# Performance work log

Hardware: AMD Instinct MI355X
Metric: run time of the kernel (lower is better)

Reference implementation:

```python
import jax, jax.numpy as jnp
import numpy as np

NUM_EMBEDDINGS = 1024
EMBEDDING_DIM = 256


def setup_inputs() -> dict:
    key = jax.random.key(0)
    k_in, k_w = jax.random.split(key)
    inputs = jax.random.normal(k_in, (32, EMBEDDING_DIM, 2048), dtype=jnp.float32)
    # nn.Embedding weight initialized uniform in [-1/K, 1/K]
    bound = 1.0 / NUM_EMBEDDINGS
    weight = jax.random.uniform(k_w, (NUM_EMBEDDINGS, EMBEDDING_DIM),
                                dtype=jnp.float32, minval=-bound, maxval=bound)
    return {"inputs": inputs, "weight": weight}


def reference(inputs, weight):
    B, D, T = inputs.shape
    # [B, D, T] -> [B*T, D]
    flat = jnp.transpose(inputs, (0, 2, 1)).reshape(-1, D)
    distances = (jnp.sum(flat * flat, axis=1, keepdims=True)
                 + jnp.sum(weight * weight, axis=1)
                 - 2.0 * flat @ weight.T)  # [N, K]
    encoding_indices = jnp.argmin(distances, axis=1)  # [N]
    # one-hot @ weight is just a gather
    quantized = weight[encoding_indices].reshape(B, T, D)  # [B, T, D]
    quantized = jnp.transpose(quantized, (0, 2, 1))  # [B, D, T]
    # straight-through estimator
    quantized = inputs + jax.lax.stop_gradient(quantized - inputs)
    return quantized, encoding_indices[:, None]
```

## Files before the change

kernel.cpp:

```cpp
#include <hip/hip_runtime.h>


#define VQ_B   32
#define VQ_D   256
#define VQ_T   2048
#define VQ_K   1024

typedef _Float16 f16x8 __attribute__((ext_vector_type(8)));
typedef float    f32x4 __attribute__((ext_vector_type(4)));

#define GLOAD_LDS16(gaddr, laddr) \
  __builtin_amdgcn_global_load_lds((const __attribute__((address_space(1))) void*)(gaddr), \
                                   (__attribute__((address_space(3))) void*)(laddr), 16, 0, 0)

__global__ void vq_wprep_kernel(const float* __restrict__ w,
                                float* __restrict__ wnorm,
                                _Float16* __restrict__ Wh,
                                _Float16* __restrict__ Wl) {
    const int k = blockIdx.x * 256 + threadIdx.x;
    const float4* wr = (const float4*)(w + (size_t)k * VQ_D);
    double s = 0.0;
    for (int i = 0; i < VQ_D / 4; ++i) {
        float4 v = wr[i];
        s += (double)v.x * v.x + (double)v.y * v.y
           + (double)v.z * v.z + (double)v.w * v.w;
        const float e4[4] = {v.x, v.y, v.z, v.w};
        #pragma unroll
        for (int j = 0; j < 4; ++j) {
            const float es = e4[j] * 1024.0f;
            const _Float16 h = (_Float16)es;
            const _Float16 l = (_Float16)((es - (float)h) * 16777216.0f);
            Wh[(size_t)k * VQ_D + i * 4 + j] = h;
            Wl[(size_t)k * VQ_D + i * 4 + j] = l;
        }
    }
    wnorm[k] = (float)s;
}

__global__ __launch_bounds__(256) void vq_xprep_kernel(
    const float* __restrict__ inp,
    _Float16* __restrict__ Xh, _Float16* __restrict__ Xl,
    float* __restrict__ xnorm)
{
    __shared__ double ps[128];
    const int tid  = threadIdx.x;
    const int t    = tid & 127;
    const int half = tid >> 7;
    const int b    = blockIdx.x >> 4;
    const int tg   = (blockIdx.x & 15) * 128 + t;
    const float* p = inp + (size_t)b * VQ_D * VQ_T + tg;

    double s = 0.0;
    for (int dc = half * 16; dc < half * 16 + 16; ++dc) {
        float x[8];
        #pragma unroll
        for (int j = 0; j < 8; ++j)
            x[j] = p[(size_t)(dc * 8 + j) * VQ_T];
        f16x8 hv, lv;
        #pragma unroll
        for (int j = 0; j < 8; ++j) {
            s += (double)x[j] * (double)x[j];
            const _Float16 h = (_Float16)x[j];
            hv[j] = h;
            lv[j] = (_Float16)((x[j] - (float)h) * 16777216.0f);
        }
        const size_t off = (((size_t)b * 32 + dc) * VQ_T + tg) * 8;
        *(f16x8*)(Xh + off) = hv;
        *(f16x8*)(Xl + off) = lv;
    }
    if (half) ps[t] = s;
    __syncthreads();
    if (!half) xnorm[(size_t)b * VQ_T + tg] = (float)(s + ps[t]);
}

__global__ __launch_bounds__(256, 2) void vq_mfma_kernel(
    const _Float16* __restrict__ Wh, const _Float16* __restrict__ Wl,
    const _Float16* __restrict__ Xh, const _Float16* __restrict__ Xl,
    const float* __restrict__ wnorm, const float* __restrict__ xnorm,
    const float* __restrict__ w,
    float* __restrict__ outq, float* __restrict__ outi)
{
    __shared__ alignas(16) char stg[2][32768];
    const int tid  = threadIdx.x;
    const int lane = tid & 63;
    const int wv   = tid >> 6;
    const int m16  = lane & 15;
    const int quad = lane >> 4;
    const int wm   = wv & 1;
    const int wn   = wv >> 1;
    const int b    = blockIdx.x >> 4;
    const int tt0  = (blockIdx.x & 15) * 128;
    const long bt  = (long)b * VQ_T + tt0;

    float xnr[4];
    #pragma unroll
    for (int fn = 0; fn < 4; ++fn)
        xnr[fn] = xnorm[bt + wn * 64 + fn * 16 + m16];

    const char* gp[8];
    #pragma unroll
    for (int i = 0; i < 8; ++i) {
        const int hf = i >> 2, f = i & 3;
        if (wv < 2) {
            const char* baseW = (const char*)((wv & 1) ? Wl : Wh);
            gp[i] = baseW + (size_t)(hf * 64 + f * 16 + m16) * 512 + quad * 16;
        } else {
            const char* baseX = (const char*)((wv & 1) ? Xl : Xh);
            gp[i] = baseX + (((size_t)b * 32 + quad) * 2048
                             + (tt0 + hf * 64 + f * 16 + m16)) * 16;
        }
    }
    auto advance = [&](int q) {
        if ((q & 7) == 7) {
            #pragma unroll
            for (int i = 0; i < 8; ++i)
                gp[i] += (wv < 2) ? (long)(65536 - 448) : (long)(-7) * 131072;
        } else {
            #pragma unroll
            for (int i = 0; i < 8; ++i)
                gp[i] += (wv < 2) ? 64L : 131072L;
        }
    };

    float bestv[4] = {3.0e38f, 3.0e38f, 3.0e38f, 3.0e38f};
    int   besti[4] = {0, 0, 0, 0};
    f32x4 acch[4][4], accl[4][4];

    #pragma unroll
    for (int i = 0; i < 8; ++i)
        GLOAD_LDS16(gp[i], &stg[0][(wv * 8 + i) * 1024]);
    advance(0);

    for (int s = 0; s < 64; ++s) {
        const int cur = s & 1;
        if ((s & 7) == 0) {
            #pragma unroll
            for (int fm = 0; fm < 4; ++fm)
                #pragma unroll
                for (int fn = 0; fn < 4; ++fn) {
                    acch[fm][fn] = (f32x4){0.f, 0.f, 0.f, 0.f};
                    accl[fm][fn] = (f32x4){0.f, 0.f, 0.f, 0.f};
                }
        }
        __syncthreads();
        if (s < 63) {
            #pragma unroll
            for (int i = 0; i < 8; ++i)
                GLOAD_LDS16(gp[i], &stg[cur ^ 1][(wv * 8 + i) * 1024]);
            advance(s + 1);
        }

        const char* base = stg[cur];
        f16x8 ah[4], al[4], bh[4], bl[4];
        #pragma unroll
        for (int f = 0; f < 4; ++f) {
            ah[f] = *(const f16x8*)(base + ((wm * 4 + f)) * 1024 + lane * 16);
            al[f] = *(const f16x8*)(base + ((8 + wm * 4 + f)) * 1024 + lane * 16);
            bh[f] = *(const f16x8*)(base + ((16 + wn * 4 + f)) * 1024 + lane * 16);
            bl[f] = *(const f16x8*)(base + ((24 + wn * 4 + f)) * 1024 + lane * 16);
        }
        #pragma unroll
        for (int fm = 0; fm < 4; ++fm)
            #pragma unroll
            for (int fn = 0; fn < 4; ++fn) {
                acch[fm][fn] = __builtin_amdgcn_mfma_f32_16x16x32_f16(
                    ah[fm], bh[fn], acch[fm][fn], 0, 0, 0);
                accl[fm][fn] = __builtin_amdgcn_mfma_f32_16x16x32_f16(
                    ah[fm], bl[fn], accl[fm][fn], 0, 0, 0);
                accl[fm][fn] = __builtin_amdgcn_mfma_f32_16x16x32_f16(
                    al[fm], bh[fn], accl[fm][fn], 0, 0, 0);
            }

        if ((s & 7) == 7) {
            const int k0 = (s >> 3) * 128;
            #pragma unroll
            for (int fm = 0; fm < 4; ++fm) {
                #pragma unroll
                for (int r = 0; r < 4; ++r) {
                    const int kg = k0 + wm * 64 + fm * 16 + quad * 4 + r;
                    const float wnk = wnorm[kg];
                    #pragma unroll
                    for (int fn = 0; fn < 4; ++fn) {
                        const float t1 = xnr[fn] + wnk;
                        const float d2 = (acch[fm][fn][r]
                                          + accl[fm][fn][r] * 5.9604644775390625e-8f)
                                         * 0.001953125f;
                        const float sc = t1 - d2;
                        if (sc < bestv[fn]) { bestv[fn] = sc; besti[fn] = kg; }
                    }
                }
            }
        }
    }

    float rv[4]; int ri[4];
    #pragma unroll
    for (int fn = 0; fn < 4; ++fn) {
        float bv = bestv[fn]; int bi = besti[fn];
        #pragma unroll
        for (int mask = 16; mask <= 32; mask <<= 1) {
            const float ov = __shfl_xor(bv, mask, 64);
            const int   oi = __shfl_xor(bi, mask, 64);
            if (ov < bv || (ov == bv && oi < bi)) { bv = ov; bi = oi; }
        }
        rv[fn] = bv; ri[fn] = bi;
    }

    __syncthreads();
    float* sv = (float*)stg[0];
    int*   si = (int*)(stg[0] + 1024);
    if (quad == 0) {
        #pragma unroll
        for (int fn = 0; fn < 4; ++fn) {
            const int tl = wn * 64 + fn * 16 + m16;
            sv[wm * 128 + tl] = rv[fn];
            si[wm * 128 + tl] = ri[fn];
        }
    }
    __syncthreads();
    if (tid < 128) {
        const float v0 = sv[tid], v1 = sv[128 + tid];
        const int   i0 = si[tid], i1 = si[128 + tid];
        const int   bi = (v1 < v0 || (v1 == v0 && i1 < i0)) ? i1 : i0;
        si[tid] = bi;
        outi[bt + tid] = (float)bi;
    }
    __syncthreads();

    {
        const int t  = tid & 127;
        const int dh = tid >> 7;
        const int bi = si[t];
        const float* wrow = w + (size_t)bi * VQ_D + dh * 128;
        float* obase = outq + ((size_t)b * VQ_D + (size_t)dh * 128) * VQ_T + tt0 + t;
        #pragma unroll 4
        for (int dd = 0; dd < 128; dd += 4) {
            float4 v = *(const float4*)(wrow + dd);
            obase[(size_t)(dd + 0) * VQ_T] = v.x;
            obase[(size_t)(dd + 1) * VQ_T] = v.y;
            obase[(size_t)(dd + 2) * VQ_T] = v.z;
            obase[(size_t)(dd + 3) * VQ_T] = v.w;
        }
    }
}

extern "C" void kernel_launch(void* const* d_in, const int* in_sizes, int n_in,
                              void* d_out, int out_size, void* d_ws, size_t ws_size,
                              hipStream_t stream) {
    const float* inp = (const float*)d_in[0];
    const float* w   = (const float*)d_in[1];
    float* outq  = (float*)d_out;
    float* outi  = outq + (size_t)VQ_B * VQ_D * VQ_T;

    float*    wnorm = (float*)d_ws;
    float*    xnorm = wnorm + VQ_K;
    _Float16* Wh    = (_Float16*)(xnorm + VQ_B * VQ_T);
    _Float16* Wl    = Wh + (size_t)VQ_K * VQ_D;
    _Float16* Xh    = Wl + (size_t)VQ_K * VQ_D;
    _Float16* Xl    = Xh + (size_t)VQ_B * VQ_T * VQ_D;

    vq_wprep_kernel<<<dim3(VQ_K / 256), dim3(256), 0, stream>>>(w, wnorm, Wh, Wl);
    vq_xprep_kernel<<<dim3(VQ_B * (VQ_T / 128)), dim3(256), 0, stream>>>(
        inp, Xh, Xl, xnorm);
    vq_mfma_kernel<<<dim3(VQ_B * (VQ_T / 128)), dim3(256), 0, stream>>>(
        Wh, Wl, Xh, Xl, wnorm, xnorm, w, outq, outi);
}
```

Baseline: 273.6 us.

## Fuse X split-precision prep into MFMA kernel and parallelize weight prep

The separate X preprocessing kernel is folded into the start of the MFMA kernel. Each block converts its own 128-token slice to fp16 hi/lo, computes the x norms into shared memory, and then streams the converted data back through global memory via the async LDS loads. The weight-prep kernel now spreads each codebook row across 16 threads with vectorized fp16 stores and a shared-memory reduction, instead of one thread per row on only 4 blocks. This removes a kernel launch and the xnorm global round trip, at the cost of relying on a threadfence for visibility of the freshly written Xh/Xl within the block.

```diff
diff --git a/kernel.cpp b/kernel.cpp
--- a/kernel.cpp
+++ b/kernel.cpp
@@ -7,76 +7,55 @@
 #define VQ_K   1024
 
 typedef _Float16 f16x8 __attribute__((ext_vector_type(8)));
+typedef _Float16 f16x4 __attribute__((ext_vector_type(4)));
 typedef float    f32x4 __attribute__((ext_vector_type(4)));
 
 #define GLOAD_LDS16(gaddr, laddr) \
   __builtin_amdgcn_global_load_lds((const __attribute__((address_space(1))) void*)(gaddr), \
                                    (__attribute__((address_space(3))) void*)(laddr), 16, 0, 0)
 
-__global__ void vq_wprep_kernel(const float* __restrict__ w,
-                                float* __restrict__ wnorm,
-                                _Float16* __restrict__ Wh,
-                                _Float16* __restrict__ Wl) {
-    const int k = blockIdx.x * 256 + threadIdx.x;
-    const float4* wr = (const float4*)(w + (size_t)k * VQ_D);
+__global__ __launch_bounds__(256) void vq_wprep_kernel(
+    const float* __restrict__ w, float* __restrict__ wnorm,
+    _Float16* __restrict__ Wh, _Float16* __restrict__ Wl) {
+    __shared__ double ws_[16][16];
+    const int tid = threadIdx.x;
+    const int kk  = tid >> 4;
+    const int dg  = tid & 15;
+    const int k   = blockIdx.x * 16 + kk;
+    const float* src = w + (size_t)k * VQ_D + dg * 16;
     double s = 0.0;
-    for (int i = 0; i < VQ_D / 4; ++i) {
-        float4 v = wr[i];
+    #pragma unroll
+    for (int q = 0; q < 4; ++q) {
+        float4 v = *(const float4*)(src + q * 4);
         s += (double)v.x * v.x + (double)v.y * v.y
            + (double)v.z * v.z + (double)v.w * v.w;
         const float e4[4] = {v.x, v.y, v.z, v.w};
+        f16x4 hv, lv;
         #pragma unroll
         for (int j = 0; j < 4; ++j) {
             const float es = e4[j] * 1024.0f;
             const _Float16 h = (_Float16)es;
-            const _Float16 l = (_Float16)((es - (float)h) * 16777216.0f);
-            Wh[(size_t)k * VQ_D + i * 4 + j] = h;
-            Wl[(size_t)k * VQ_D + i * 4 + j] = l;
-        }
-    }
-    wnorm[k] = (float)s;
+            hv[j] = h;
+            lv[j] = (_Float16)((es - (float)h) * 16777216.0f);
+        }
+        *(f16x4*)(Wh + (size_t)k * VQ_D + dg * 16 + q * 4) = hv;
+        *(f16x4*)(Wl + (size_t)k * VQ_D + dg * 16 + q * 4) = lv;
+    }
+    ws_[kk][dg] = s;
+    __syncthreads();
+    if (dg == 0) {
+        double acc = 0.0;
+        #pragma unroll
+        for (int g = 0; g < 16; ++g) acc += ws_[kk][g];
+        wnorm[k] = (float)acc;
+    }
 }
 
-__global__ __launch_bounds__(256) void vq_xprep_kernel(
+__global__ __launch_bounds__(256, 2) void vq_mfma_kernel(
     const float* __restrict__ inp,
+    const _Float16* __restrict__ Wh, const _Float16* __restrict__ Wl,
     _Float16* __restrict__ Xh, _Float16* __restrict__ Xl,
-    float* __restrict__ xnorm)
-{
-    __shared__ double ps[128];
-    const int tid  = threadIdx.x;
-    const int t    = tid & 127;
-    const int half = tid >> 7;
-    const int b    = blockIdx.x >> 4;
-    const int tg   = (blockIdx.x & 15) * 128 + t;
-    const float* p = inp + (size_t)b * VQ_D * VQ_T + tg;
-
-    double s = 0.0;
-    for (int dc = half * 16; dc < half * 16 + 16; ++dc) {
-        float x[8];
-        #pragma unroll
-        for (int j = 0; j < 8; ++j)
-            x[j] = p[(size_t)(dc * 8 + j) * VQ_T];
-        f16x8 hv, lv;
-        #pragma unroll
-        for (int j = 0; j < 8; ++j) {
-            s += (double)x[j] * (double)x[j];
-            const _Float16 h = (_Float16)x[j];
-            hv[j] = h;
-            lv[j] = (_Float16)((x[j] - (float)h) * 16777216.0f);
-        }
-        const size_t off = (((size_t)b * 32 + dc) * VQ_T + tg) * 8;
-        *(f16x8*)(Xh + off) = hv;
-        *(f16x8*)(Xl + off) = lv;
-    }
-    if (half) ps[t] = s;
-    __syncthreads();
-    if (!half) xnorm[(size_t)b * VQ_T + tg] = (float)(s + ps[t]);
-}
-
-__global__ __launch_bounds__(256, 2) void vq_mfma_kernel(
-    const _Float16* __restrict__ Wh, const _Float16* __restrict__ Wl,
-    const _Float16* __restrict__ Xh, const _Float16* __restrict__ Xl,
-    const float* __restrict__ wnorm, const float* __restrict__ xnorm,
+    const float* __restrict__ wnorm,
     const float* __restrict__ w,
     float* __restrict__ outq, float* __restrict__ outi)
 {
@@ -92,10 +71,46 @@
     const int tt0  = (blockIdx.x & 15) * 128;
     const long bt  = (long)b * VQ_T + tt0;
 
+    {
+        const int t    = tid & 127;
+        const int half = tid >> 7;
+        const float* p = inp + (size_t)b * VQ_D * VQ_T + tt0 + t;
+        double s = 0.0;
+        #pragma unroll 4
+        for (int dc = half * 16; dc < half * 16 + 16; ++dc) {
+            float x[8];
+            #pragma unroll
+            for (int j = 0; j < 8; ++j)
+                x[j] = p[(size_t)(dc * 8 + j) * VQ_T];
+            f16x8 hv, lv;
+            #pragma unroll
+            for (int j = 0; j < 8; ++j) {
+                s += (double)x[j] * (double)x[j];
+                const _Float16 h = (_Float16)x[j];
+                hv[j] = h;
+                lv[j] = (_Float16)((x[j] - (float)h) * 16777216.0f);
+            }
+            const size_t off = (((size_t)b * 32 + dc) * VQ_T + tt0 + t) * 8;
+            *(f16x8*)(Xh + off) = hv;
+            *(f16x8*)(Xl + off) = lv;
+        }
+        double* ps  = (double*)stg[0];
+        float*  xns = (float*)(stg[0] + 1024);
+        if (half) ps[t] = s;
+        __threadfence();
+        __syncthreads();
+        if (!half) xns[t] = (float)(s + ps[t]);
+        __syncthreads();
+    }
+
     float xnr[4];
-    #pragma unroll
-    for (int fn = 0; fn < 4; ++fn)
-        xnr[fn] = xnorm[bt + wn * 64 + fn * 16 + m16];
+    {
+        const float* xns = (const float*)(stg[0] + 1024);
+        #pragma unroll
+        for (int fn = 0; fn < 4; ++fn)
+            xnr[fn] = xns[wn * 64 + fn * 16 + m16];
+    }
+    __syncthreads();
 
     const char* gp[8];
     #pragma unroll
@@ -253,15 +268,12 @@
     float* outi  = outq + (size_t)VQ_B * VQ_D * VQ_T;
 
     float*    wnorm = (float*)d_ws;
-    float*    xnorm = wnorm + VQ_K;
-    _Float16* Wh    = (_Float16*)(xnorm + VQ_B * VQ_T);
+    _Float16* Wh    = (_Float16*)(wnorm + VQ_K);
     _Float16* Wl    = Wh + (size_t)VQ_K * VQ_D;
     _Float16* Xh    = Wl + (size_t)VQ_K * VQ_D;
     _Float16* Xl    = Xh + (size_t)VQ_B * VQ_T * VQ_D;
 
-    vq_wprep_kernel<<<dim3(VQ_K / 256), dim3(256), 0, stream>>>(w, wnorm, Wh, Wl);
-    vq_xprep_kernel<<<dim3(VQ_B * (VQ_T / 128)), dim3(256), 0, stream>>>(
-        inp, Xh, Xl, xnorm);
+    vq_wprep_kernel<<<dim3(VQ_K / 16), dim3(256), 0, stream>>>(w, wnorm, Wh, Wl);
     vq_mfma_kernel<<<dim3(VQ_B * (VQ_T / 128)), dim3(256), 0, stream>>>(
-        Wh, Wl, Xh, Xl, wnorm, xnorm, w, outq, outi);
+        inp, Wh, Wl, Xh, Xl, wnorm, w, outq, outi);
 }
```

Measured after the change: 325.3 us. +18.9%, slower.
